# Kernel optimization log

Hardware: AMD Instinct MI355X
Metric: run time of the kernel (lower is better)

Reference implementation:

```python
import jax, jax.numpy as jnp
import numpy as np

# Scaled-down LLaMA-style decoder with per-layer memory K/V prefix (tokenmix2 Decoder)
L, D, H, Dh, F, V = 2, 4096, 32, 128, 8192, 8192
B, S, M = 1, 1024, 512
EPS = 1e-5
ROPE_BASE = 10000.0


def setup_inputs() -> dict:
    key = jax.random.key(0)
    ks = jax.random.split(key, 16)
    sd = D ** -0.5
    sf = F ** -0.5
    n = lambda k, shape, s: (jax.random.normal(k, shape, jnp.float32) * s)
    return {
        "input_ids": jax.random.randint(ks[0], (B, S), 0, V),
        "memory": jax.random.normal(ks[1], (L, B, M, D), jnp.float32),
        "embed": n(ks[2], (V, D), sd),
        "Wq": n(ks[3], (L, D, D), sd),
        "Wk": n(ks[4], (L, D, D), sd),
        "Wv": n(ks[5], (L, D, D), sd),
        "Wo": n(ks[6], (L, D, D), sd),
        "Wg": n(ks[7], (L, F, D), sd),
        "Wu": n(ks[8], (L, F, D), sd),
        "Wd": n(ks[9], (L, D, F), sf),
        "Wmk": n(ks[10], (L, D, D), sd),
        "Wmv": n(ks[11], (L, D, D), sd),
        "ln1": jnp.ones((L, D), jnp.float32),
        "ln2": jnp.ones((L, D), jnp.float32),
        "normw": jnp.ones((D,), jnp.float32),
        "lm_head": n(ks[12], (V, D), sd),
    }


def _rms(x, w):
    return x * jax.lax.rsqrt(jnp.mean(x * x, axis=-1, keepdims=True) + EPS) * w


def _rot_half(x):
    x1, x2 = jnp.split(x, 2, axis=-1)
    return jnp.concatenate([-x2, x1], axis=-1)


def _rope_tables(n_pos):
    inv_freq = 1.0 / (ROPE_BASE ** (jnp.arange(0, Dh, 2, dtype=jnp.float32) / Dh))
    ang = jnp.arange(n_pos, dtype=jnp.float32)[:, None] * inv_freq[None, :]
    emb = jnp.concatenate([ang, ang], axis=-1)  # [n_pos, Dh]
    return jnp.cos(emb), jnp.sin(emb)


def reference(input_ids, memory, embed, Wq, Wk, Wv, Wo, Wg, Wu, Wd, Wmk, Wmv,
              ln1, ln2, normw, lm_head):
    h = embed[input_ids]                                   # [B,S,D]
    cos, sin = _rope_tables(M + S)                         # memory tokens sit at positions 0..M
    cos_k, sin_k = cos[None, None], sin[None, None]        # [1,1,M+S,Dh]
    cos_q, sin_q = cos[None, None, M:], sin[None, None, M:]  # queries at positions M..M+S
    qpos = jnp.arange(M, M + S)
    kpos = jnp.arange(M + S)
    mask = qpos[:, None] >= kpos[None, :]                  # causal incl. full memory prefix
    scale = Dh ** -0.5

    def heads(x, T):
        return x.reshape(B, T, H, Dh).transpose(0, 2, 1, 3)  # [B,H,T,Dh]

    for l in range(L):
        x = _rms(h, ln1[l])
        q = heads(x @ Wq[l].T, S)
        k = heads(x @ Wk[l].T, S)
        v = heads(x @ Wv[l].T, S)
        mk = heads(memory[l] @ Wmk[l].T, M)
        mv = heads(memory[l] @ Wmv[l].T, M)
        K = jnp.concatenate([mk, k], axis=2)               # [B,H,M+S,Dh]
        Vv = jnp.concatenate([mv, v], axis=2)
        q = q * cos_q + _rot_half(q) * sin_q
        K = K * cos_k + _rot_half(K) * sin_k
        scores = jnp.einsum('bhqd,bhkd->bhqk', q, K) * scale
        scores = jnp.where(mask, scores, jnp.float32(-1e30))
        p = jax.nn.softmax(scores, axis=-1)
        o = jnp.einsum('bhqk,bhkd->bhqd', p, Vv)
        o = o.transpose(0, 2, 1, 3).reshape(B, S, D)
        h = h + o @ Wo[l].T
        x = _rms(h, ln2[l])
        h = h + (jax.nn.silu(x @ Wg[l].T) * (x @ Wu[l].T)) @ Wd[l].T

    h = _rms(h, normw)
    logits = (h @ lm_head.T).astype(jnp.float32)           # [B,S,V]
    return logits
```

## Files before the change

### kernel.cpp

```cpp
#include <hip/hip_runtime.h>
#include <hip/hip_bf16.h>

typedef unsigned int uint;
typedef unsigned short u16;

#define D_ 4096
#define H_ 32
#define DH 128
#define F_ 8192
#define V_ 8192
#define S_ 1024
#define M_ 512
#define L_ 2
#define KV_ (M_ + S_)

typedef __attribute__((ext_vector_type(8))) short s16x8;
typedef __attribute__((ext_vector_type(4))) float f32x4;
typedef __attribute__((ext_vector_type(4))) u16 u16x4;

__device__ __forceinline__ u16 f2bf(float f) {
    uint u = __float_as_uint(f);
    u += 0x7FFFu + ((u >> 16) & 1u);
    return (u16)(u >> 16);
}
__device__ __forceinline__ float bf2f(u16 h) {
    return __uint_as_float(((uint)h) << 16);
}
__device__ __forceinline__ void gload_lds16(const void* g, void* l) {
    __builtin_amdgcn_global_load_lds(
        (const __attribute__((address_space(1))) unsigned int*)g,
        (__attribute__((address_space(3))) unsigned int*)l, 16, 0, 0);
}

__global__ void k_embed(const int* __restrict__ ids, const float* __restrict__ embed,
                        float* __restrict__ h) {
    int row = blockIdx.x;
    const float4* src = (const float4*)(embed + (size_t)ids[row] * D_);
    float4* dst = (float4*)(h + (size_t)row * D_);
    for (int i = threadIdx.x; i < D_ / 4; i += 256) dst[i] = src[i];
}

__global__ __launch_bounds__(256) void k_rms(const float* __restrict__ hin,
                                             const float* __restrict__ w,
                                             u16* __restrict__ out) {
    int row = blockIdx.x, t = threadIdx.x;
    const float4* src = (const float4*)(hin + (size_t)row * D_);
    float4 v[4];
    float ss = 0.f;
#pragma unroll
    for (int i = 0; i < 4; ++i) {
        v[i] = src[t + 256 * i];
        ss += v[i].x * v[i].x + v[i].y * v[i].y + v[i].z * v[i].z + v[i].w * v[i].w;
    }
#pragma unroll
    for (int off = 32; off; off >>= 1) ss += __shfl_xor(ss, off);
    __shared__ float red[4];
    if ((t & 63) == 0) red[t >> 6] = ss;
    __syncthreads();
    float tot = red[0] + red[1] + red[2] + red[3];
    float sc = rsqrtf(tot * (1.0f / D_) + 1e-5f);
    const float4* wp = (const float4*)w;
    u16x4* op = (u16x4*)(out + (size_t)row * D_);
#pragma unroll
    for (int i = 0; i < 4; ++i) {
        float4 wv = wp[t + 256 * i];
        u16x4 o;
        o[0] = f2bf(v[i].x * sc * wv.x);
        o[1] = f2bf(v[i].y * sc * wv.y);
        o[2] = f2bf(v[i].z * sc * wv.z);
        o[3] = f2bf(v[i].w * sc * wv.w);
        op[t + 256 * i] = o;
    }
}

__global__ void k_cvt(const float* __restrict__ src, u16* __restrict__ dst, int n4) {
    int i = blockIdx.x * 256 + threadIdx.x;
    if (i < n4) {
        float4 v = ((const float4*)src)[i];
        u16x4 o;
        o[0] = f2bf(v.x); o[1] = f2bf(v.y); o[2] = f2bf(v.z); o[3] = f2bf(v.w);
        ((u16x4*)dst)[i] = o;
    }
}

__global__ void k_silu(const u16* __restrict__ G, const u16* __restrict__ U,
                       u16* __restrict__ out, int n8) {
    int i = blockIdx.x * 256 + threadIdx.x;
    if (i < n8) {
        s16x8 g = ((const s16x8*)G)[i];
        s16x8 u = ((const s16x8*)U)[i];
        s16x8 o;
#pragma unroll
        for (int j = 0; j < 8; ++j) {
            float gv = bf2f((u16)g[j]), uv = bf2f((u16)u[j]);
            o[j] = (short)f2bf(gv / (1.0f + __expf(-gv)) * uv);
        }
        ((s16x8*)out)[i] = o;
    }
}

__global__ void k_ropetab(float* __restrict__ tab) {
    int pos = blockIdx.x, i = threadIdx.x;
    float invf = powf(10000.0f, -(float)i * (1.0f / 64.0f));
    float ang = (float)pos * invf;
    tab[(size_t)pos * 128 + i * 2] = cosf(ang);
    tab[(size_t)pos * 128 + i * 2 + 1] = sinf(ang);
}

__global__ __launch_bounds__(256) void k_rope(u16* __restrict__ buf,
                                              const float* __restrict__ tab, int pos0) {
    int row = blockIdx.x, t = threadIdx.x;
    const float2* tp = (const float2*)(tab + (size_t)(pos0 + row) * 128);
    u16* p = buf + (size_t)row * D_;
#pragma unroll
    for (int j = 0; j < 8; ++j) {
        int pid = t + 256 * j;
        int hd = pid >> 6, i = pid & 63;
        float2 cs = tp[i];
        int base = hd * 128 + i;
        float v0 = bf2f(p[base]), v1 = bf2f(p[base + 64]);
        p[base] = f2bf(v0 * cs.x - v1 * cs.y);
        p[base + 64] = f2bf(v1 * cs.x + v0 * cs.y);
    }
}

__global__ __launch_bounds__(256) void k_transpose(const u16* __restrict__ src,
                                                   u16* __restrict__ dst) {
    __shared__ u16 tile[64][66];
    int tc = blockIdx.x * 64;
    int tr = blockIdx.y * 64;
    int t = threadIdx.x;
    int c = t & 63, r0 = t >> 6;
#pragma unroll
    for (int i = 0; i < 16; ++i) {
        int r = r0 + i * 4;
        tile[r][c] = src[(size_t)(tr + r) * D_ + tc + c];
    }
    __syncthreads();
#pragma unroll
    for (int i = 0; i < 16; ++i) {
        int r = r0 + i * 4;
        dst[(size_t)(tc + r) * KV_ + tr + c] = tile[c][r];
    }
}

struct GemmB8 {
    const u16* A[5];
    const u16* B[5];
    void* O[5];
    int mrows[5];
};

template <int EPI>
__global__ __launch_bounds__(512, 2) void k_gemm8(GemmB8 P, int Nn, int Kfull) {
    int z = blockIdx.z;
    size_t bm = blockIdx.y, bn = blockIdx.x;
    if ((int)(bm * 256) >= P.mrows[z]) return;
    const u16* A = P.A[z];
    const u16* Bw = P.B[z];
    __shared__ __align__(16) u16 AB[2][2][2][128][64];

    const int tid = threadIdx.x;
    const int lane = tid & 63, wid = tid >> 6;
    const int l16 = lane & 15, lh = lane >> 4;
    const int wrow = (wid >> 2) * 64;
    const int wcol = (wid & 3) * 32;
    const int nt = Kfull >> 6;

    const int grow0 = tid >> 3;
    const int gsw = ((tid & 7) ^ (grow0 & 7)) * 8;
    const u16* pA = A + (size_t)(bm * 256 + grow0) * Kfull + gsw;
    const u16* pB = Bw + (size_t)(bn * 256 + grow0) * Kfull + gsw;

    auto stage = [&](const u16* base, int mat, int h, int t) {
        if (t >= nt) return;
        const u16* g = base + (size_t)(h * 128) * Kfull + t * 64;
        u16* l = &AB[t & 1][mat][h][0][0] + tid * 8;
        gload_lds16(g, l);
        gload_lds16(g + (size_t)64 * Kfull, l + 4096);
    };

    f32x4 acc[4][4][2];
#pragma unroll
    for (int q = 0; q < 4; ++q)
#pragma unroll
        for (int mf = 0; mf < 4; ++mf)
#pragma unroll
            for (int nf = 0; nf < 2; ++nf)
#pragma unroll
                for (int e = 0; e < 4; ++e) acc[q][mf][nf][e] = 0.f;

    stage(pA, 0, 0, 0); stage(pB, 1, 0, 0);
    stage(pA, 0, 1, 0); stage(pB, 1, 1, 0);
    stage(pA, 0, 0, 1); stage(pB, 1, 0, 1);
    asm volatile("s_waitcnt vmcnt(4)" ::: "memory");
    __builtin_amdgcn_s_barrier();
    asm volatile("" ::: "memory");

    for (int T = 0; T < nt; ++T) {
        const int cb = T & 1;
        s16x8 af[4][2], bb[2][2];

#pragma unroll
        for (int kk = 0; kk < 2; ++kk) {
            const int sw = ((kk * 4 + lh) ^ (l16 & 7)) * 8;
#pragma unroll
            for (int mf = 0; mf < 4; ++mf)
                af[mf][kk] = *(const s16x8*)(&AB[cb][0][0][wrow + mf * 16 + l16][sw]);
#pragma unroll
            for (int nf = 0; nf < 2; ++nf)
                bb[nf][kk] = *(const s16x8*)(&AB[cb][1][0][wcol + nf * 16 + l16][sw]);
        }
        stage(pA, 0, 1, T + 1);
        asm volatile("" ::: "memory");
        __builtin_amdgcn_s_barrier();
        asm volatile("" ::: "memory");
        __builtin_amdgcn_s_setprio(1);
#pragma unroll
        for (int kk = 0; kk < 2; ++kk)
#pragma unroll
            for (int mf = 0; mf < 4; ++mf)
#pragma unroll
                for (int nf = 0; nf < 2; ++nf)
                    acc[0][mf][nf] = __builtin_amdgcn_mfma_f32_16x16x32_bf16(
                        af[mf][kk], bb[nf][kk], acc[0][mf][nf], 0, 0, 0);
        __builtin_amdgcn_s_setprio(0);
        asm volatile("" ::: "memory");
        __builtin_amdgcn_s_barrier();
        asm volatile("" ::: "memory");

#pragma unroll
        for (int kk = 0; kk < 2; ++kk) {
            const int sw = ((kk * 4 + lh) ^ (l16 & 7)) * 8;
#pragma unroll
            for (int nf = 0; nf < 2; ++nf)
                bb[nf][kk] = *(const s16x8*)(&AB[cb][1][1][wcol + nf * 16 + l16][sw]);
        }
        stage(pB, 1, 1, T + 1);
        asm volatile("" ::: "memory");
        __builtin_amdgcn_s_barrier();
        asm volatile("" ::: "memory");
        __builtin_amdgcn_s_setprio(1);
#pragma unroll
        for (int kk = 0; kk < 2; ++kk)
#pragma unroll
            for (int mf = 0; mf < 4; ++mf)
#pragma unroll
                for (int nf = 0; nf < 2; ++nf)
                    acc[1][mf][nf] = __builtin_amdgcn_mfma_f32_16x16x32_bf16(
                        af[mf][kk], bb[nf][kk], acc[1][mf][nf], 0, 0, 0);
        __builtin_amdgcn_s_setprio(0);
        asm volatile("" ::: "memory");
        __builtin_amdgcn_s_barrier();
        asm volatile("" ::: "memory");

#pragma unroll
        for (int kk = 0; kk < 2; ++kk) {
            const int sw = ((kk * 4 + lh) ^ (l16 & 7)) * 8;
#pragma unroll
            for (int mf = 0; mf < 4; ++mf)
                af[mf][kk] = *(const s16x8*)(&AB[cb][0][1][wrow + mf * 16 + l16][sw]);
#pragma unroll
            for (int nf = 0; nf < 2; ++nf)
                bb[nf][kk] = *(const s16x8*)(&AB[cb][1][0][wcol + nf * 16 + l16][sw]);
        }
        stage(pA, 0, 0, T + 2);
        asm volatile("" ::: "memory");
        __builtin_amdgcn_s_barrier();
        asm volatile("" ::: "memory");
        __builtin_amdgcn_s_setprio(1);
#pragma unroll
        for (int kk = 0; kk < 2; ++kk)
#pragma unroll
            for (int mf = 0; mf < 4; ++mf)
#pragma unroll
                for (int nf = 0; nf < 2; ++nf)
                    acc[2][mf][nf] = __builtin_amdgcn_mfma_f32_16x16x32_bf16(
                        af[mf][kk], bb[nf][kk], acc[2][mf][nf], 0, 0, 0);
        __builtin_amdgcn_s_setprio(0);
        asm volatile("" ::: "memory");
        __builtin_amdgcn_s_barrier();
        asm volatile("" ::: "memory");

#pragma unroll
        for (int kk = 0; kk < 2; ++kk) {
            const int sw = ((kk * 4 + lh) ^ (l16 & 7)) * 8;
#pragma unroll
            for (int nf = 0; nf < 2; ++nf)
                bb[nf][kk] = *(const s16x8*)(&AB[cb][1][1][wcol + nf * 16 + l16][sw]);
        }
        stage(pB, 1, 0, T + 2);
        asm volatile("" ::: "memory");
        __builtin_amdgcn_s_barrier();
        asm volatile("" ::: "memory");
        __builtin_amdgcn_s_setprio(1);
#pragma unroll
        for (int kk = 0; kk < 2; ++kk)
#pragma unroll
            for (int mf = 0; mf < 4; ++mf)
#pragma unroll
                for (int nf = 0; nf < 2; ++nf)
                    acc[3][mf][nf] = __builtin_amdgcn_mfma_f32_16x16x32_bf16(
                        af[mf][kk], bb[nf][kk], acc[3][mf][nf], 0, 0, 0);
        __builtin_amdgcn_s_setprio(0);
        if (T < nt - 2) asm volatile("s_waitcnt vmcnt(4)" ::: "memory");
        else if (T == nt - 2) asm volatile("s_waitcnt vmcnt(0)" ::: "memory");
        asm volatile("" ::: "memory");
        __builtin_amdgcn_s_barrier();
        asm volatile("" ::: "memory");
    }

    void* Oo = P.O[z];
#pragma unroll
    for (int q = 0; q < 4; ++q) {
        const int qm = q >> 1, qn = q & 1;
#pragma unroll
        for (int mf = 0; mf < 4; ++mf) {
#pragma unroll
            for (int nf = 0; nf < 2; ++nf) {
#pragma unroll
                for (int rr = 0; rr < 4; ++rr) {
                    int grow = (int)bm * 256 + qm * 128 + wrow + mf * 16 + lh * 4 + rr;
                    int gcol = (int)bn * 256 + qn * 128 + wcol + nf * 16 + l16;
                    size_t idx = (size_t)grow * Nn + gcol;
                    float v = acc[q][mf][nf][rr];
                    if constexpr (EPI == 0) ((u16*)Oo)[idx] = f2bf(v);
                    else ((float*)Oo)[idx] = v;
                }
            }
        }
    }
}

struct GemmB2 {
    const u16* A[5];
    const u16* B[5];
    void* O[5];
    int mrows[5];
    int koff[5];
};

template <int EPI>
__global__ __launch_bounds__(256) void k_gemm2(GemmB2 P, int Nn, int Kstep, int Kfull) {
    int z = blockIdx.z;
    size_t bm = blockIdx.y, bn = blockIdx.x;
    if ((int)(bm * 128) >= P.mrows[z]) return;
    const u16* A = P.A[z];
    const u16* Bw = P.B[z];
    int koff = P.koff[z];
    __shared__ __align__(16) u16 As[128 * 64];
    __shared__ __align__(16) u16 Bs[128 * 64];
    int tid = threadIdx.x;
    int lane = tid & 63, wid = tid >> 6;
    int l16 = lane & 15, lh = lane >> 4;
    int wm = (wid >> 1) * 64, wn = (wid & 1) * 64;

    const u16 *pA[4], *pB[4];
    int ldso[4];
#pragma unroll
    for (int i = 0; i < 4; ++i) {
        int c = tid + 256 * i;
        int r = c >> 3, s = c & 7;
        int ssw = (s ^ (r & 7)) * 8;
        pA[i] = A + (size_t)(bm * 128 + r) * Kfull + koff + ssw;
        pB[i] = Bw + (size_t)(bn * 128 + r) * Kfull + koff + ssw;
        ldso[i] = c * 8;
    }

    f32x4 acc[4][4];
#pragma unroll
    for (int i = 0; i < 4; ++i)
#pragma unroll
        for (int j = 0; j < 4; ++j)
#pragma unroll
            for (int e = 0; e < 4; ++e) acc[i][j][e] = 0.f;

    int nt = Kstep >> 6;
    for (int t = 0; t < nt; ++t) {
        int k0 = t << 6;
#pragma unroll
        for (int i = 0; i < 4; ++i) gload_lds16(pA[i] + k0, &As[ldso[i]]);
#pragma unroll
        for (int i = 0; i < 4; ++i) gload_lds16(pB[i] + k0, &Bs[ldso[i]]);
        __syncthreads();
#pragma unroll
        for (int kk = 0; kk < 2; ++kk) {
            int sidx = kk * 4 + lh;
            int sw = (sidx ^ (l16 & 7)) * 8;
            s16x8 af[4], bf4[4];
#pragma unroll
            for (int mi = 0; mi < 4; ++mi)
                af[mi] = *(const s16x8*)(&As[(wm + mi * 16 + l16) * 64 + sw]);
#pragma unroll
            for (int ni = 0; ni < 4; ++ni)
                bf4[ni] = *(const s16x8*)(&Bs[(wn + ni * 16 + l16) * 64 + sw]);
#pragma unroll
            for (int mi = 0; mi < 4; ++mi)
#pragma unroll
                for (int ni = 0; ni < 4; ++ni)
                    acc[mi][ni] = __builtin_amdgcn_mfma_f32_16x16x32_bf16(
                        af[mi], bf4[ni], acc[mi][ni], 0, 0, 0);
        }
        __syncthreads();
    }

    void* Oo = P.O[z];
#pragma unroll
    for (int mi = 0; mi < 4; ++mi) {
#pragma unroll
        for (int ni = 0; ni < 4; ++ni) {
#pragma unroll
            for (int r = 0; r < 4; ++r) {
                int grow = (int)bm * 128 + wm + mi * 16 + lh * 4 + r;
                int gcol = (int)bn * 128 + wn + ni * 16 + l16;
                size_t idx = (size_t)grow * Nn + gcol;
                float v = acc[mi][ni][r];
                if constexpr (EPI == 1) ((float*)Oo)[idx] = v;
                else atomicAdd((float*)Oo + idx, v);
            }
        }
    }
}

__global__ __launch_bounds__(64) void k_attn(const u16* __restrict__ Qb,
                                             const u16* __restrict__ Kb,
                                             const u16* __restrict__ VT,
                                             u16* __restrict__ Ob) {
    int qt = blockIdx.x, hd = blockIdx.y;
    int lane = threadIdx.x, l16 = lane & 15, lh = lane >> 4;
    __shared__ __align__(16) float Pl[16 * 36];

    s16x8 qf[4];
#pragma unroll
    for (int c = 0; c < 4; ++c)
        qf[c] = *(const s16x8*)(Qb + (size_t)(qt * 16 + l16) * D_ + hd * DH + c * 32 + lh * 8);

    f32x4 o[8];
#pragma unroll
    for (int dc = 0; dc < 8; ++dc)
#pragma unroll
        for (int e = 0; e < 4; ++e) o[dc][e] = 0.f;
    float m[4], lsum[4];
#pragma unroll
    for (int r = 0; r < 4; ++r) { m[r] = -1e30f; lsum[r] = 0.f; }

    const float scale = 0.08838834764831845f;
    int qbase = M_ + qt * 16;
    int nkb = (M_ + qt * 16 + 16 + 31) >> 5;

    for (int kb = 0; kb < nkb; ++kb) {
        f32x4 s0, s1;
#pragma unroll
        for (int e = 0; e < 4; ++e) { s0[e] = 0.f; s1[e] = 0.f; }
#pragma unroll
        for (int c = 0; c < 4; ++c) {
            s16x8 kf0 = *(const s16x8*)(Kb + (size_t)(kb * 32 + l16) * D_ + hd * DH + c * 32 + lh * 8);
            s16x8 kf1 = *(const s16x8*)(Kb + (size_t)(kb * 32 + 16 + l16) * D_ + hd * DH + c * 32 + lh * 8);
            s0 = __builtin_amdgcn_mfma_f32_16x16x32_bf16(qf[c], kf0, s0, 0, 0, 0);
            s1 = __builtin_amdgcn_mfma_f32_16x16x32_bf16(qf[c], kf1, s1, 0, 0, 0);
        }
        int kp0 = kb * 32 + l16, kp1 = kp0 + 16;
        float pm[4];
#pragma unroll
        for (int r = 0; r < 4; ++r) {
            int qp = qbase + lh * 4 + r;
            float v0 = s0[r] * scale; if (kp0 > qp) v0 = -1e30f;
            float v1 = s1[r] * scale; if (kp1 > qp) v1 = -1e30f;
            s0[r] = v0; s1[r] = v1;
            pm[r] = fmaxf(v0, v1);
        }
#pragma unroll
        for (int r = 0; r < 4; ++r) {
#pragma unroll
            for (int off = 8; off; off >>= 1) pm[r] = fmaxf(pm[r], __shfl_xor(pm[r], off));
        }
        float alpha[4];
#pragma unroll
        for (int r = 0; r < 4; ++r) {
            float mn = fmaxf(m[r], pm[r]);
            alpha[r] = __expf(m[r] - mn);
            m[r] = mn;
            float p0 = __expf(s0[r] - mn), p1 = __expf(s1[r] - mn);
            s0[r] = p0; s1[r] = p1;
            float t = p0 + p1;
#pragma unroll
            for (int off = 8; off; off >>= 1) t += __shfl_xor(t, off);
            lsum[r] = lsum[r] * alpha[r] + t;
        }
#pragma unroll
        for (int r = 0; r < 4; ++r) {
            Pl[(lh * 4 + r) * 36 + l16] = s0[r];
            Pl[(lh * 4 + r) * 36 + 16 + l16] = s1[r];
        }
        __syncthreads();
        s16x8 pf;
        {
            const f32x4* pp = (const f32x4*)(Pl + l16 * 36 + lh * 8);
            f32x4 a = pp[0], b = pp[1];
            pf[0] = (short)f2bf(a[0]); pf[1] = (short)f2bf(a[1]);
            pf[2] = (short)f2bf(a[2]); pf[3] = (short)f2bf(a[3]);
            pf[4] = (short)f2bf(b[0]); pf[5] = (short)f2bf(b[1]);
            pf[6] = (short)f2bf(b[2]); pf[7] = (short)f2bf(b[3]);
        }
        __syncthreads();
#pragma unroll
        for (int dc = 0; dc < 8; ++dc) {
#pragma unroll
            for (int r = 0; r < 4; ++r) o[dc][r] *= alpha[r];
        }
#pragma unroll
        for (int dc = 0; dc < 8; ++dc) {
            s16x8 vf = *(const s16x8*)(VT + (size_t)(hd * DH + dc * 16 + l16) * KV_ + kb * 32 + lh * 8);
            o[dc] = __builtin_amdgcn_mfma_f32_16x16x32_bf16(pf, vf, o[dc], 0, 0, 0);
        }
    }
#pragma unroll
    for (int dc = 0; dc < 8; ++dc) {
#pragma unroll
        for (int r = 0; r < 4; ++r) {
            float val = o[dc][r] / lsum[r];
            Ob[(size_t)(qt * 16 + lh * 4 + r) * D_ + hd * DH + dc * 16 + l16] = f2bf(val);
        }
    }
}

extern "C" void kernel_launch(void* const* d_in, const int* in_sizes, int n_in,
                              void* d_out, int out_size, void* d_ws, size_t ws_size,
                              hipStream_t stream) {
    const int* ids = (const int*)d_in[0];
    const float* memory = (const float*)d_in[1];
    const float* embed = (const float*)d_in[2];
    const float* Wq = (const float*)d_in[3];
    const float* Wk = (const float*)d_in[4];
    const float* Wv = (const float*)d_in[5];
    const float* Wo = (const float*)d_in[6];
    const float* Wg = (const float*)d_in[7];
    const float* Wu = (const float*)d_in[8];
    const float* Wd = (const float*)d_in[9];
    const float* Wmk = (const float*)d_in[10];
    const float* Wmv = (const float*)d_in[11];
    const float* ln1 = (const float*)d_in[12];
    const float* ln2 = (const float*)d_in[13];
    const float* normw = (const float*)d_in[14];
    const float* lm = (const float*)d_in[15];

    char* ws = (char*)d_ws;
    float* h   = (float*)(ws + 0x0000000);
    u16* xb    = (u16*)(ws + 0x1000000);
    float* tab = (float*)(ws + 0x1800000);
    u16* memb  = (u16*)(ws + 0x1900000);
    u16* Qb    = (u16*)(ws + 0x1E00000);
    u16* Kb    = (u16*)(ws + 0x2600000);
    u16* Vb    = (u16*)(ws + 0x3200000);
    u16* VT    = (u16*)(ws + 0x3E00000);
    u16* Ob    = (u16*)(ws + 0x4A00000);
    u16* Gb16  = (u16*)(ws + 0x1E00000);
    u16* Ub16  = (u16*)(ws + 0x2E00000);
    u16* tb    = (u16*)(ws + 0x3E00000);
    u16* Wqb  = (u16*)(ws + 0x07000000);
    u16* Wkb  = (u16*)(ws + 0x0B000000);
    u16* Wvb  = (u16*)(ws + 0x0F000000);
    u16* Wob  = (u16*)(ws + 0x13000000);
    u16* Wmkb = (u16*)(ws + 0x17000000);
    u16* Wmvb = (u16*)(ws + 0x1B000000);
    u16* Wgb  = (u16*)(ws + 0x1F000000);
    u16* Wub  = (u16*)(ws + 0x27000000);
    u16* Wdb  = (u16*)(ws + 0x2F000000);
    u16* lmb  = (u16*)(ws + 0x37000000);

    const int nDD = L_ * D_ * D_ / 4, nFD = L_ * F_ * D_ / 4, nVD = V_ * D_ / 4;
    k_cvt<<<(nDD + 255) / 256, 256, 0, stream>>>(Wq, Wqb, nDD);
    k_cvt<<<(nDD + 255) / 256, 256, 0, stream>>>(Wk, Wkb, nDD);
    k_cvt<<<(nDD + 255) / 256, 256, 0, stream>>>(Wv, Wvb, nDD);
    k_cvt<<<(nDD + 255) / 256, 256, 0, stream>>>(Wo, Wob, nDD);
    k_cvt<<<(nDD + 255) / 256, 256, 0, stream>>>(Wmk, Wmkb, nDD);
    k_cvt<<<(nDD + 255) / 256, 256, 0, stream>>>(Wmv, Wmvb, nDD);
    k_cvt<<<(nFD + 255) / 256, 256, 0, stream>>>(Wg, Wgb, nFD);
    k_cvt<<<(nFD + 255) / 256, 256, 0, stream>>>(Wu, Wub, nFD);
    k_cvt<<<(nFD + 255) / 256, 256, 0, stream>>>(Wd, Wdb, nFD);
    k_cvt<<<(nVD + 255) / 256, 256, 0, stream>>>(lm, lmb, nVD);

    k_embed<<<S_, 256, 0, stream>>>(ids, embed, h);
    k_ropetab<<<KV_, 64, 0, stream>>>(tab);

    for (int l = 0; l < L_; ++l) {
        const size_t oDD = (size_t)l * D_ * D_;
        const size_t oFD = (size_t)l * F_ * D_;

        k_rms<<<S_, 256, 0, stream>>>(h, ln1 + l * D_, xb);
        k_cvt<<<(M_ * D_ / 4 + 255) / 256, 256, 0, stream>>>(
            memory + (size_t)l * M_ * D_, memb, M_ * D_ / 4);

        GemmB8 g1{};
        g1.A[0] = xb;   g1.B[0] = Wqb + oDD;  g1.O[0] = Qb;                    g1.mrows[0] = S_;
        g1.A[1] = xb;   g1.B[1] = Wkb + oDD;  g1.O[1] = Kb + (size_t)M_ * D_;  g1.mrows[1] = S_;
        g1.A[2] = xb;   g1.B[2] = Wvb + oDD;  g1.O[2] = Vb + (size_t)M_ * D_;  g1.mrows[2] = S_;
        g1.A[3] = memb; g1.B[3] = Wmkb + oDD; g1.O[3] = Kb;                    g1.mrows[3] = M_;
        g1.A[4] = memb; g1.B[4] = Wmvb + oDD; g1.O[4] = Vb;                    g1.mrows[4] = M_;
        k_gemm8<0><<<dim3(D_ / 256, S_ / 256, 5), 512, 0, stream>>>(g1, D_, D_);

        k_rope<<<S_, 256, 0, stream>>>(Qb, tab, M_);
        k_rope<<<KV_, 256, 0, stream>>>(Kb, tab, 0);
        k_transpose<<<dim3(D_ / 64, KV_ / 64), 256, 0, stream>>>(Vb, VT);
        k_attn<<<dim3(S_ / 16, H_), 64, 0, stream>>>(Qb, Kb, VT, Ob);

        GemmB2 g2{};
        g2.A[0] = Ob; g2.B[0] = Wob + oDD; g2.O[0] = h; g2.mrows[0] = S_; g2.koff[0] = 0;
        g2.A[1] = Ob; g2.B[1] = Wob + oDD; g2.O[1] = h; g2.mrows[1] = S_; g2.koff[1] = 2048;
        k_gemm2<4><<<dim3(D_ / 128, S_ / 128, 2), 256, 0, stream>>>(g2, D_, 2048, D_);

        k_rms<<<S_, 256, 0, stream>>>(h, ln2 + l * D_, xb);
        GemmB8 g3{};
        g3.A[0] = xb; g3.B[0] = Wgb + oFD; g3.O[0] = Gb16; g3.mrows[0] = S_;
        g3.A[1] = xb; g3.B[1] = Wub + oFD; g3.O[1] = Ub16; g3.mrows[1] = S_;
        k_gemm8<0><<<dim3(F_ / 256, S_ / 256, 2), 512, 0, stream>>>(g3, F_, D_);
        k_silu<<<(S_ * F_ / 8 + 255) / 256, 256, 0, stream>>>(Gb16, Ub16, tb, S_ * F_ / 8);
        GemmB2 g5{};
        g5.A[0] = tb; g5.B[0] = Wdb + oFD; g5.O[0] = h; g5.mrows[0] = S_; g5.koff[0] = 0;
        g5.A[1] = tb; g5.B[1] = Wdb + oFD; g5.O[1] = h; g5.mrows[1] = S_; g5.koff[1] = 4096;
        k_gemm2<4><<<dim3(D_ / 128, S_ / 128, 2), 256, 0, stream>>>(g5, D_, 4096, F_);
    }

    k_rms<<<S_, 256, 0, stream>>>(h, normw, xb);
    GemmB2 g6{};
    g6.A[0] = xb; g6.B[0] = lmb; g6.O[0] = (float*)d_out; g6.mrows[0] = S_; g6.koff[0] = 0;
    k_gemm2<1><<<dim3(V_ / 128, S_ / 128, 1), 256, 0, stream>>>(g6, V_, D_, D_);
}
```

Measured before the change: 1.885 ms.

## Route Wo, down-proj and lm_head GEMMs through 256x256 split-K gemm8 kernel

Removes the 128x128 k_gemm2 kernel and extends the pipelined 256x256 gemm8 kernel with a K offset, a K-step parameter and an atomicAdd epilogue. The Wo and down projections now use a 4-way K split, and lm_head uses a 2-way split with atomics into an output that is zeroed up front. The larger tiles aim to raise operand reuse and let these GEMMs benefit from the double-buffered pipeline. In exchange the change adds more fp32 atomic traffic, an extra pass to zero the output, and nondeterministic summation order.

```diff
diff --git a/kernel.cpp b/kernel.cpp
--- a/kernel.cpp
+++ b/kernel.cpp
@@ -32,6 +32,11 @@
         (__attribute__((address_space(3))) unsigned int*)l, 16, 0, 0);
 }
 
+__global__ void k_zero(float* __restrict__ dst, int n4) {
+    int i = blockIdx.x * 256 + threadIdx.x;
+    if (i < n4) ((float4*)dst)[i] = make_float4(0.f, 0.f, 0.f, 0.f);
+}
+
 __global__ void k_embed(const int* __restrict__ ids, const float* __restrict__ embed,
                         float* __restrict__ h) {
     int row = blockIdx.x;
@@ -149,15 +154,17 @@
     const u16* B[5];
     void* O[5];
     int mrows[5];
+    int koff[5];
 };
 
 template <int EPI>
-__global__ __launch_bounds__(512, 2) void k_gemm8(GemmB8 P, int Nn, int Kfull) {
+__global__ __launch_bounds__(512, 2) void k_gemm8(GemmB8 P, int Nn, int Kstep, int Kfull) {
     int z = blockIdx.z;
     size_t bm = blockIdx.y, bn = blockIdx.x;
     if ((int)(bm * 256) >= P.mrows[z]) return;
     const u16* A = P.A[z];
     const u16* Bw = P.B[z];
+    const int koff = P.koff[z];
     __shared__ __align__(16) u16 AB[2][2][2][128][64];
 
     const int tid = threadIdx.x;
@@ -165,12 +172,12 @@
     const int l16 = lane & 15, lh = lane >> 4;
     const int wrow = (wid >> 2) * 64;
     const int wcol = (wid & 3) * 32;
-    const int nt = Kfull >> 6;
+    const int nt = Kstep >> 6;
 
     const int grow0 = tid >> 3;
     const int gsw = ((tid & 7) ^ (grow0 & 7)) * 8;
-    const u16* pA = A + (size_t)(bm * 256 + grow0) * Kfull + gsw;
-    const u16* pB = Bw + (size_t)(bn * 256 + grow0) * Kfull + gsw;
+    const u16* pA = A + (size_t)(bm * 256 + grow0) * Kfull + koff + gsw;
+    const u16* pB = Bw + (size_t)(bn * 256 + grow0) * Kfull + koff + gsw;
 
     auto stage = [&](const u16* base, int mat, int h, int t) {
         if (t >= nt) return;
@@ -325,98 +332,9 @@
                     size_t idx = (size_t)grow * Nn + gcol;
                     float v = acc[q][mf][nf][rr];
                     if constexpr (EPI == 0) ((u16*)Oo)[idx] = f2bf(v);
-                    else ((float*)Oo)[idx] = v;
+                    else if constexpr (EPI == 1) ((float*)Oo)[idx] = v;
+                    else atomicAdd((float*)Oo + idx, v);
                 }
-            }
-        }
-    }
-}
-
-struct GemmB2 {
-    const u16* A[5];
-    const u16* B[5];
-    void* O[5];
-    int mrows[5];
-    int koff[5];
-};
-
-template <int EPI>
-__global__ __launch_bounds__(256) void k_gemm2(GemmB2 P, int Nn, int Kstep, int Kfull) {
-    int z = blockIdx.z;
-    size_t bm = blockIdx.y, bn = blockIdx.x;
-    if ((int)(bm * 128) >= P.mrows[z]) return;
-    const u16* A = P.A[z];
-    const u16* Bw = P.B[z];
-    int koff = P.koff[z];
-    __shared__ __align__(16) u16 As[128 * 64];
-    __shared__ __align__(16) u16 Bs[128 * 64];
-    int tid = threadIdx.x;
-    int lane = tid & 63, wid = tid >> 6;
-    int l16 = lane & 15, lh = lane >> 4;
-    int wm = (wid >> 1) * 64, wn = (wid & 1) * 64;
-
-    const u16 *pA[4], *pB[4];
-    int ldso[4];
-#pragma unroll
-    for (int i = 0; i < 4; ++i) {
-        int c = tid + 256 * i;
-        int r = c >> 3, s = c & 7;
-        int ssw = (s ^ (r & 7)) * 8;
-        pA[i] = A + (size_t)(bm * 128 + r) * Kfull + koff + ssw;
-        pB[i] = Bw + (size_t)(bn * 128 + r) * Kfull + koff + ssw;
-        ldso[i] = c * 8;
-    }
-
-    f32x4 acc[4][4];
-#pragma unroll
-    for (int i = 0; i < 4; ++i)
-#pragma unroll
-        for (int j = 0; j < 4; ++j)
-#pragma unroll
-            for (int e = 0; e < 4; ++e) acc[i][j][e] = 0.f;
-
-    int nt = Kstep >> 6;
-    for (int t = 0; t < nt; ++t) {
-        int k0 = t << 6;
-#pragma unroll
-        for (int i = 0; i < 4; ++i) gload_lds16(pA[i] + k0, &As[ldso[i]]);
-#pragma unroll
-        for (int i = 0; i < 4; ++i) gload_lds16(pB[i] + k0, &Bs[ldso[i]]);
-        __syncthreads();
-#pragma unroll
-        for (int kk = 0; kk < 2; ++kk) {
-            int sidx = kk * 4 + lh;
-            int sw = (sidx ^ (l16 & 7)) * 8;
-            s16x8 af[4], bf4[4];
-#pragma unroll
-            for (int mi = 0; mi < 4; ++mi)
-                af[mi] = *(const s16x8*)(&As[(wm + mi * 16 + l16) * 64 + sw]);
-#pragma unroll
-            for (int ni = 0; ni < 4; ++ni)
-                bf4[ni] = *(const s16x8*)(&Bs[(wn + ni * 16 + l16) * 64 + sw]);
-#pragma unroll
-            for (int mi = 0; mi < 4; ++mi)
-#pragma unroll
-                for (int ni = 0; ni < 4; ++ni)
-                    acc[mi][ni] = __builtin_amdgcn_mfma_f32_16x16x32_bf16(
-                        af[mi], bf4[ni], acc[mi][ni], 0, 0, 0);
-        }
-        __syncthreads();
-    }
-
-    void* Oo = P.O[z];
-#pragma unroll
-    for (int mi = 0; mi < 4; ++mi) {
-#pragma unroll
-        for (int ni = 0; ni < 4; ++ni) {
-#pragma unroll
-            for (int r = 0; r < 4; ++r) {
-                int grow = (int)bm * 128 + wm + mi * 16 + lh * 4 + r;
-                int gcol = (int)bn * 128 + wn + ni * 16 + l16;
-                size_t idx = (size_t)grow * Nn + gcol;
-                float v = acc[mi][ni][r];
-                if constexpr (EPI == 1) ((float*)Oo)[idx] = v;
-                else atomicAdd((float*)Oo + idx, v);
             }
         }
     }
@@ -580,6 +498,7 @@
     k_cvt<<<(nFD + 255) / 256, 256, 0, stream>>>(Wd, Wdb, nFD);
     k_cvt<<<(nVD + 255) / 256, 256, 0, stream>>>(lm, lmb, nVD);
 
+    k_zero<<<(S_ * V_ / 4 + 255) / 256, 256, 0, stream>>>((float*)d_out, S_ * V_ / 4);
     k_embed<<<S_, 256, 0, stream>>>(ids, embed, h);
     k_ropetab<<<KV_, 64, 0, stream>>>(tab);
 
@@ -597,32 +516,39 @@
         g1.A[2] = xb;   g1.B[2] = Wvb + oDD;  g1.O[2] = Vb + (size_t)M_ * D_;  g1.mrows[2] = S_;
         g1.A[3] = memb; g1.B[3] = Wmkb + oDD; g1.O[3] = Kb;                    g1.mrows[3] = M_;
         g1.A[4] = memb; g1.B[4] = Wmvb + oDD; g1.O[4] = Vb;                    g1.mrows[4] = M_;
-        k_gemm8<0><<<dim3(D_ / 256, S_ / 256, 5), 512, 0, stream>>>(g1, D_, D_);
+        k_gemm8<0><<<dim3(D_ / 256, S_ / 256, 5), 512, 0, stream>>>(g1, D_, D_, D_);
 
         k_rope<<<S_, 256, 0, stream>>>(Qb, tab, M_);
         k_rope<<<KV_, 256, 0, stream>>>(Kb, tab, 0);
         k_transpose<<<dim3(D_ / 64, KV_ / 64), 256, 0, stream>>>(Vb, VT);
         k_attn<<<dim3(S_ / 16, H_), 64, 0, stream>>>(Qb, Kb, VT, Ob);
 
-        GemmB2 g2{};
-        g2.A[0] = Ob; g2.B[0] = Wob + oDD; g2.O[0] = h; g2.mrows[0] = S_; g2.koff[0] = 0;
-        g2.A[1] = Ob; g2.B[1] = Wob + oDD; g2.O[1] = h; g2.mrows[1] = S_; g2.koff[1] = 2048;
-        k_gemm2<4><<<dim3(D_ / 128, S_ / 128, 2), 256, 0, stream>>>(g2, D_, 2048, D_);
+        GemmB8 g2{};
+        for (int s = 0; s < 4; ++s) {
+            g2.A[s] = Ob; g2.B[s] = Wob + oDD; g2.O[s] = h;
+            g2.mrows[s] = S_; g2.koff[s] = s * 1024;
+        }
+        k_gemm8<2><<<dim3(D_ / 256, S_ / 256, 4), 512, 0, stream>>>(g2, D_, 1024, D_);
 
         k_rms<<<S_, 256, 0, stream>>>(h, ln2 + l * D_, xb);
         GemmB8 g3{};
         g3.A[0] = xb; g3.B[0] = Wgb + oFD; g3.O[0] = Gb16; g3.mrows[0] = S_;
         g3.A[1] = xb; g3.B[1] = Wub + oFD; g3.O[1] = Ub16; g3.mrows[1] = S_;
-        k_gemm8<0><<<dim3(F_ / 256, S_ / 256, 2), 512, 0, stream>>>(g3, F_, D_);
+        k_gemm8<0><<<dim3(F_ / 256, S_ / 256, 2), 512, 0, stream>>>(g3, F_, D_, D_);
         k_silu<<<(S_ * F_ / 8 + 255) / 256, 256, 0, stream>>>(Gb16, Ub16, tb, S_ * F_ / 8);
-        GemmB2 g5{};
-        g5.A[0] = tb; g5.B[0] = Wdb + oFD; g5.O[0] = h; g5.mrows[0] = S_; g5.koff[0] = 0;
-        g5.A[1] = tb; g5.B[1] = Wdb + oFD; g5.O[1] = h; g5.mrows[1] = S_; g5.koff[1] = 4096;
-        k_gemm2<4><<<dim3(D_ / 128, S_ / 128, 2), 256, 0, stream>>>(g5, D_, 4096, F_);
+        GemmB8 g5{};
+        for (int s = 0; s < 4; ++s) {
+            g5.A[s] = tb; g5.B[s] = Wdb + oFD; g5.O[s] = h;
+            g5.mrows[s] = S_; g5.koff[s] = s * 2048;
+        }
+        k_gemm8<2><<<dim3(D_ / 256, S_ / 256, 4), 512, 0, stream>>>(g5, D_, 2048, F_);
     }
 
     k_rms<<<S_, 256, 0, stream>>>(h, normw, xb);
-    GemmB2 g6{};
-    g6.A[0] = xb; g6.B[0] = lmb; g6.O[0] = (float*)d_out; g6.mrows[0] = S_; g6.koff[0] = 0;
-    k_gemm2<1><<<dim3(V_ / 128, S_ / 128, 1), 256, 0, stream>>>(g6, V_, D_, D_);
-}
+    GemmB8 g6{};
+    for (int s = 0; s < 2; ++s) {
+        g6.A[s] = xb; g6.B[s] = lmb; g6.O[s] = (float*)d_out;
+        g6.mrows[s] = S_; g6.koff[s] = s * 2048;
+    }
+    k_gemm8<2><<<dim3(V_ / 256, S_ / 256, 2), 512, 0, stream>>>(g6, V_, 2048, D_);
+}
```

Result: no change. 1.917 ms (+1.7%).

## Replace atomic split-K reductions with partial buffers fused into residual-add RMSNorm

Applied to the files above, without the earlier changes.

Split-K GEMMs now write two partial outputs to separate buffers instead of atomically adding into the residual. A new kernel sums the partials into the residual and computes the next RMSNorm in one pass. The LM head also gets a two-way split-K followed by an add kernel. Weight conversion is merged into one batched launch and the Q/K RoPE launches into one. This removes float atomics and some launches, at the cost of extra partial-buffer traffic and extra workspace.

```diff
diff --git a/kernel.cpp b/kernel.cpp
--- a/kernel.cpp
+++ b/kernel.cpp
@@ -73,6 +73,75 @@
     }
 }
 
+__global__ __launch_bounds__(256) void k_addrms(float* __restrict__ hio,
+                                                const float* __restrict__ p0,
+                                                const float* __restrict__ p1,
+                                                const float* __restrict__ w,
+                                                u16* __restrict__ out) {
+    int row = blockIdx.x, t = threadIdx.x;
+    float4* hp = (float4*)(hio + (size_t)row * D_);
+    const float4* q0 = (const float4*)(p0 + (size_t)row * D_);
+    const float4* q1 = (const float4*)(p1 + (size_t)row * D_);
+    float4 v[4];
+    float ss = 0.f;
+#pragma unroll
+    for (int i = 0; i < 4; ++i) {
+        float4 a = hp[t + 256 * i];
+        float4 b = q0[t + 256 * i];
+        float4 c = q1[t + 256 * i];
+        v[i].x = a.x + b.x + c.x; v[i].y = a.y + b.y + c.y;
+        v[i].z = a.z + b.z + c.z; v[i].w = a.w + b.w + c.w;
+        hp[t + 256 * i] = v[i];
+        ss += v[i].x * v[i].x + v[i].y * v[i].y + v[i].z * v[i].z + v[i].w * v[i].w;
+    }
+#pragma unroll
+    for (int off = 32; off; off >>= 1) ss += __shfl_xor(ss, off);
+    __shared__ float red[4];
+    if ((t & 63) == 0) red[t >> 6] = ss;
+    __syncthreads();
+    float tot = red[0] + red[1] + red[2] + red[3];
+    float sc = rsqrtf(tot * (1.0f / D_) + 1e-5f);
+    const float4* wp = (const float4*)w;
+    u16x4* op = (u16x4*)(out + (size_t)row * D_);
+#pragma unroll
+    for (int i = 0; i < 4; ++i) {
+        float4 wv = wp[t + 256 * i];
+        u16x4 o;
+        o[0] = f2bf(v[i].x * sc * wv.x);
+        o[1] = f2bf(v[i].y * sc * wv.y);
+        o[2] = f2bf(v[i].z * sc * wv.z);
+        o[3] = f2bf(v[i].w * sc * wv.w);
+        op[t + 256 * i] = o;
+    }
+}
+
+__global__ void k_add2(const float* __restrict__ p0, const float* __restrict__ p1,
+                       float* __restrict__ dst, int n4) {
+    int i = blockIdx.x * 256 + threadIdx.x;
+    if (i < n4) {
+        float4 a = ((const float4*)p0)[i];
+        float4 b = ((const float4*)p1)[i];
+        ((float4*)dst)[i] = make_float4(a.x + b.x, a.y + b.y, a.z + b.z, a.w + b.w);
+    }
+}
+
+struct CvtBatch {
+    const float* src[10];
+    u16* dst[10];
+    int off[11];
+};
+__global__ void k_cvtall(CvtBatch C, int total4) {
+    int i = blockIdx.x * 256 + threadIdx.x;
+    if (i >= total4) return;
+    int s = 0;
+    while (i >= C.off[s + 1]) ++s;
+    int j = i - C.off[s];
+    float4 v = ((const float4*)C.src[s])[j];
+    u16x4 o;
+    o[0] = f2bf(v.x); o[1] = f2bf(v.y); o[2] = f2bf(v.z); o[3] = f2bf(v.w);
+    ((u16x4*)C.dst[s])[j] = o;
+}
+
 __global__ void k_cvt(const float* __restrict__ src, u16* __restrict__ dst, int n4) {
     int i = blockIdx.x * 256 + threadIdx.x;
     if (i < n4) {
@@ -107,11 +176,14 @@
     tab[(size_t)pos * 128 + i * 2 + 1] = sinf(ang);
 }
 
-__global__ __launch_bounds__(256) void k_rope(u16* __restrict__ buf,
-                                              const float* __restrict__ tab, int pos0) {
-    int row = blockIdx.x, t = threadIdx.x;
-    const float2* tp = (const float2*)(tab + (size_t)(pos0 + row) * 128);
-    u16* p = buf + (size_t)row * D_;
+__global__ __launch_bounds__(256) void k_rope2(u16* __restrict__ Qb, u16* __restrict__ Kb,
+                                               const float* __restrict__ tab) {
+    int b = blockIdx.x, t = threadIdx.x;
+    u16* p;
+    int pos;
+    if (b < S_) { p = Qb + (size_t)b * D_; pos = M_ + b; }
+    else        { p = Kb + (size_t)(b - S_) * D_; pos = b - S_; }
+    const float2* tp = (const float2*)(tab + (size_t)pos * 128);
 #pragma unroll
     for (int j = 0; j < 8; ++j) {
         int pid = t + 256 * j;
@@ -414,9 +486,7 @@
                 int grow = (int)bm * 128 + wm + mi * 16 + lh * 4 + r;
                 int gcol = (int)bn * 128 + wn + ni * 16 + l16;
                 size_t idx = (size_t)grow * Nn + gcol;
-                float v = acc[mi][ni][r];
-                if constexpr (EPI == 1) ((float*)Oo)[idx] = v;
-                else atomicAdd((float*)Oo + idx, v);
+                ((float*)Oo)[idx] = acc[mi][ni][r];
             }
         }
     }
@@ -557,37 +627,43 @@
     u16* Gb16  = (u16*)(ws + 0x1E00000);
     u16* Ub16  = (u16*)(ws + 0x2E00000);
     u16* tb    = (u16*)(ws + 0x3E00000);
-    u16* Wqb  = (u16*)(ws + 0x07000000);
-    u16* Wkb  = (u16*)(ws + 0x0B000000);
-    u16* Wvb  = (u16*)(ws + 0x0F000000);
-    u16* Wob  = (u16*)(ws + 0x13000000);
-    u16* Wmkb = (u16*)(ws + 0x17000000);
-    u16* Wmvb = (u16*)(ws + 0x1B000000);
-    u16* Wgb  = (u16*)(ws + 0x1F000000);
-    u16* Wub  = (u16*)(ws + 0x27000000);
-    u16* Wdb  = (u16*)(ws + 0x2F000000);
-    u16* lmb  = (u16*)(ws + 0x37000000);
+    float* P0  = (float*)(ws + 0x52000000 - 0x4D000000);
+    P0         = (float*)(ws + 0x5200000);
+    float* P1  = (float*)(ws + 0x6200000);
+    float* PL0 = (float*)(ws + 0x1E00000);
+    float* PL1 = (float*)(ws + 0x3E00000);
+    u16* Wqb  = (u16*)(ws + 0x08000000);
+    u16* Wkb  = (u16*)(ws + 0x0C000000);
+    u16* Wvb  = (u16*)(ws + 0x10000000);
+    u16* Wob  = (u16*)(ws + 0x14000000);
+    u16* Wmkb = (u16*)(ws + 0x18000000);
+    u16* Wmvb = (u16*)(ws + 0x1C000000);
+    u16* Wgb  = (u16*)(ws + 0x20000000);
+    u16* Wub  = (u16*)(ws + 0x28000000);
+    u16* Wdb  = (u16*)(ws + 0x30000000);
+    u16* lmb  = (u16*)(ws + 0x38000000);
 
     const int nDD = L_ * D_ * D_ / 4, nFD = L_ * F_ * D_ / 4, nVD = V_ * D_ / 4;
-    k_cvt<<<(nDD + 255) / 256, 256, 0, stream>>>(Wq, Wqb, nDD);
-    k_cvt<<<(nDD + 255) / 256, 256, 0, stream>>>(Wk, Wkb, nDD);
-    k_cvt<<<(nDD + 255) / 256, 256, 0, stream>>>(Wv, Wvb, nDD);
-    k_cvt<<<(nDD + 255) / 256, 256, 0, stream>>>(Wo, Wob, nDD);
-    k_cvt<<<(nDD + 255) / 256, 256, 0, stream>>>(Wmk, Wmkb, nDD);
-    k_cvt<<<(nDD + 255) / 256, 256, 0, stream>>>(Wmv, Wmvb, nDD);
-    k_cvt<<<(nFD + 255) / 256, 256, 0, stream>>>(Wg, Wgb, nFD);
-    k_cvt<<<(nFD + 255) / 256, 256, 0, stream>>>(Wu, Wub, nFD);
-    k_cvt<<<(nFD + 255) / 256, 256, 0, stream>>>(Wd, Wdb, nFD);
-    k_cvt<<<(nVD + 255) / 256, 256, 0, stream>>>(lm, lmb, nVD);
+    CvtBatch C{};
+    const float* srcs[10] = {Wq, Wk, Wv, Wo, Wmk, Wmv, Wg, Wu, Wd, lm};
+    u16* dsts[10] = {Wqb, Wkb, Wvb, Wob, Wmkb, Wmvb, Wgb, Wub, Wdb, lmb};
+    int ns[10] = {nDD, nDD, nDD, nDD, nDD, nDD, nFD, nFD, nFD, nVD};
+    int acc0 = 0;
+    for (int s = 0; s < 10; ++s) {
+        C.src[s] = srcs[s]; C.dst[s] = dsts[s];
+        C.off[s] = acc0; acc0 += ns[s];
+    }
+    C.off[10] = acc0;
+    k_cvtall<<<(acc0 + 255) / 256, 256, 0, stream>>>(C, acc0);
 
     k_embed<<<S_, 256, 0, stream>>>(ids, embed, h);
     k_ropetab<<<KV_, 64, 0, stream>>>(tab);
+    k_rms<<<S_, 256, 0, stream>>>(h, ln1, xb);
 
     for (int l = 0; l < L_; ++l) {
         const size_t oDD = (size_t)l * D_ * D_;
         const size_t oFD = (size_t)l * F_ * D_;
 
-        k_rms<<<S_, 256, 0, stream>>>(h, ln1 + l * D_, xb);
         k_cvt<<<(M_ * D_ / 4 + 255) / 256, 256, 0, stream>>>(
             memory + (size_t)l * M_ * D_, memb, M_ * D_ / 4);
 
@@ -599,30 +675,33 @@
         g1.A[4] = memb; g1.B[4] = Wmvb + oDD; g1.O[4] = Vb;                    g1.mrows[4] = M_;
         k_gemm8<0><<<dim3(D_ / 256, S_ / 256, 5), 512, 0, stream>>>(g1, D_, D_);
 
-        k_rope<<<S_, 256, 0, stream>>>(Qb, tab, M_);
-        k_rope<<<KV_, 256, 0, stream>>>(Kb, tab, 0);
+        k_rope2<<<S_ + KV_, 256, 0, stream>>>(Qb, Kb, tab);
         k_transpose<<<dim3(D_ / 64, KV_ / 64), 256, 0, stream>>>(Vb, VT);
         k_attn<<<dim3(S_ / 16, H_), 64, 0, stream>>>(Qb, Kb, VT, Ob);
 
         GemmB2 g2{};
-        g2.A[0] = Ob; g2.B[0] = Wob + oDD; g2.O[0] = h; g2.mrows[0] = S_; g2.koff[0] = 0;
-        g2.A[1] = Ob; g2.B[1] = Wob + oDD; g2.O[1] = h; g2.mrows[1] = S_; g2.koff[1] = 2048;
-        k_gemm2<4><<<dim3(D_ / 128, S_ / 128, 2), 256, 0, stream>>>(g2, D_, 2048, D_);
-
-        k_rms<<<S_, 256, 0, stream>>>(h, ln2 + l * D_, xb);
+        g2.A[0] = Ob; g2.B[0] = Wob + oDD; g2.O[0] = P0; g2.mrows[0] = S_; g2.koff[0] = 0;
+        g2.A[1] = Ob; g2.B[1] = Wob + oDD; g2.O[1] = P1; g2.mrows[1] = S_; g2.koff[1] = 2048;
+        k_gemm2<1><<<dim3(D_ / 128, S_ / 128, 2), 256, 0, stream>>>(g2, D_, 2048, D_);
+        k_addrms<<<S_, 256, 0, stream>>>(h, P0, P1, ln2 + l * D_, xb);
+
         GemmB8 g3{};
         g3.A[0] = xb; g3.B[0] = Wgb + oFD; g3.O[0] = Gb16; g3.mrows[0] = S_;
         g3.A[1] = xb; g3.B[1] = Wub + oFD; g3.O[1] = Ub16; g3.mrows[1] = S_;
         k_gemm8<0><<<dim3(F_ / 256, S_ / 256, 2), 512, 0, stream>>>(g3, F_, D_);
         k_silu<<<(S_ * F_ / 8 + 255) / 256, 256, 0, stream>>>(Gb16, Ub16, tb, S_ * F_ / 8);
+
         GemmB2 g5{};
-        g5.A[0] = tb; g5.B[0] = Wdb + oFD; g5.O[0] = h; g5.mrows[0] = S_; g5.koff[0] = 0;
-        g5.A[1] = tb; g5.B[1] = Wdb + oFD; g5.O[1] = h; g5.mrows[1] = S_; g5.koff[1] = 4096;
-        k_gemm2<4><<<dim3(D_ / 128, S_ / 128, 2), 256, 0, stream>>>(g5, D_, 4096, F_);
-    }
-
-    k_rms<<<S_, 256, 0, stream>>>(h, normw, xb);
+        g5.A[0] = tb; g5.B[0] = Wdb + oFD; g5.O[0] = P0; g5.mrows[0] = S_; g5.koff[0] = 0;
+        g5.A[1] = tb; g5.B[1] = Wdb + oFD; g5.O[1] = P1; g5.mrows[1] = S_; g5.koff[1] = 4096;
+        k_gemm2<1><<<dim3(D_ / 128, S_ / 128, 2), 256, 0, stream>>>(g5, D_, 4096, F_);
+        const float* nw = (l + 1 < L_) ? (ln1 + (l + 1) * D_) : normw;
+        k_addrms<<<S_, 256, 0, stream>>>(h, P0, P1, nw, xb);
+    }
+
     GemmB2 g6{};
-    g6.A[0] = xb; g6.B[0] = lmb; g6.O[0] = (float*)d_out; g6.mrows[0] = S_; g6.koff[0] = 0;
-    k_gemm2<1><<<dim3(V_ / 128, S_ / 128, 1), 256, 0, stream>>>(g6, V_, D_, D_);
-}
+    g6.A[0] = xb; g6.B[0] = lmb; g6.O[0] = PL0; g6.mrows[0] = S_; g6.koff[0] = 0;
+    g6.A[1] = xb; g6.B[1] = lmb; g6.O[1] = PL1; g6.mrows[1] = S_; g6.koff[1] = 2048;
+    k_gemm2<1><<<dim3(V_ / 128, S_ / 128, 2), 256, 0, stream>>>(g6, V_, 2048, D_);
+    k_add2<<<(S_ * V_ / 4 + 255) / 256, 256, 0, stream>>>(PL0, PL1, (float*)d_out, S_ * V_ / 4);
+}
```

Result: no change. 1.889 ms (+0.2%).
